# Kernel tuning notes

Hardware: AMD Instinct MI355X
Metric: run time of the kernel (lower is better)

## Reference

```python
import jax, jax.numpy as jnp
import numpy as np

EPS = 1e-6
N_NODES, N_EDGES, HIDDEN, NUM_HEADS = 50000, 800000, 256, 8
HEAD_DIM = HIDDEN // NUM_HEADS
MLP_HIDDEN = 4 * HIDDEN


def _ln(x):
    # LayerNorm without affine, eps=1e-6
    m = x.mean(-1, keepdims=True)
    v = ((x - m) ** 2).mean(-1, keepdims=True)
    return (x - m) * jax.lax.rsqrt(v + EPS)


def _modulate(x, shift, scale):
    return x * (1.0 + scale) + shift


def setup_inputs() -> dict:
    key = jax.random.key(0)
    ks = jax.random.split(key, 20)
    s = 0.02
    inp = {
        "x": jax.random.normal(ks[0], (N_NODES, HIDDEN), jnp.float32),
        "c": jax.random.normal(ks[1], (N_NODES, HIDDEN), jnp.float32),
        "edge_index": jax.random.randint(ks[2], (2, N_EDGES), 0, N_NODES, jnp.int64),
        "Wq": jax.random.normal(ks[3], (HIDDEN, HIDDEN), jnp.float32) * s,
        "bq": jnp.zeros((HIDDEN,), jnp.float32),
        "Wk": jax.random.normal(ks[4], (HIDDEN, HIDDEN), jnp.float32) * s,
        "bk": jnp.zeros((HIDDEN,), jnp.float32),
        "Wv": jax.random.normal(ks[5], (HIDDEN, HIDDEN), jnp.float32) * s,
        "bv": jnp.zeros((HIDDEN,), jnp.float32),
        "Wo": jax.random.normal(ks[6], (HIDDEN, HIDDEN), jnp.float32) * s,
        "bo": jnp.zeros((HIDDEN,), jnp.float32),
        "W1": jax.random.normal(ks[7], (HIDDEN, MLP_HIDDEN), jnp.float32) * s,
        "b1": jnp.zeros((MLP_HIDDEN,), jnp.float32),
        "W2": jax.random.normal(ks[8], (MLP_HIDDEN, HIDDEN), jnp.float32) * s,
        "b2": jnp.zeros((HIDDEN,), jnp.float32),
        "Wc": jax.random.normal(ks[9], (HIDDEN, 6 * HIDDEN), jnp.float32) * s,
        "bc": jnp.zeros((6 * HIDDEN,), jnp.float32),
    }
    return inp


def reference(x, c, edge_index, Wq, bq, Wk, bk, Wv, bv, Wo, bo, W1, b1, W2, b2, Wc, bc):
    n = x.shape[0]
    src, dst = edge_index[0], edge_index[1]  # messages flow src(j) -> dst(i)

    # adaLN modulation: SiLU -> Linear -> chunk 6 along feature dim
    mod = jax.nn.silu(c) @ Wc + bc  # [N, 6*H]
    shift_msa, scale_msa, gate_msa, shift_mlp, scale_mlp, gate_mlp = jnp.split(mod, 6, axis=1)

    # ---- attention branch ----
    h = _modulate(_ln(x), shift_msa, scale_msa)  # [N, HIDDEN]
    q = (h @ Wq + bq).reshape(n, NUM_HEADS, HEAD_DIM)
    k = (h @ Wk + bk).reshape(n, NUM_HEADS, HEAD_DIM)
    v = (h @ Wv + bv).reshape(n, NUM_HEADS, HEAD_DIM)

    scale = HEAD_DIM ** -0.5
    sim = jnp.einsum('ehd,ehd->eh', q[dst], k[src]) * scale  # [E, NH]
    # segment softmax over destination node
    smax = jax.ops.segment_max(sim, dst, num_segments=n)  # [N, NH]
    expd = jnp.exp(sim - smax[dst])
    denom = jax.ops.segment_sum(expd, dst, num_segments=n)  # [N, NH]
    attn = expd / denom[dst]  # [E, NH]

    msg = v[src] * attn[:, :, None]  # [E, NH, HD]
    agg = jax.ops.segment_sum(msg, dst, num_segments=n).reshape(n, HIDDEN)
    attn_out = agg @ Wo + bo

    x = x + gate_msa * attn_out

    # ---- MLP branch ----
    h2 = _modulate(_ln(x), shift_mlp, scale_mlp)
    h2 = jax.nn.gelu(h2 @ W1 + b1, approximate=True)
    mlp_out = h2 @ W2 + b2

    return x + gate_mlp * mlp_out
```

## Files before the change

### kernel.cpp

```cpp
#include <hip/hip_runtime.h>


typedef __attribute__((ext_vector_type(8))) short bf16x8;
typedef __attribute__((ext_vector_type(2))) _Float16 h2_t;
typedef __attribute__((ext_vector_type(4))) float f32x4;

__device__ __forceinline__ float bf2f(unsigned short u) {
  union { float f; unsigned int i; } x; x.i = ((unsigned int)u) << 16; return x.f;
}
__device__ __forceinline__ unsigned short f2bf(float f) {
  union { float f; unsigned int i; } x; x.f = f;
  unsigned int r = x.i + 0x7fffu + ((x.i >> 16) & 1u);
  return (unsigned short)(r >> 16);
}
__device__ __forceinline__ float sigm_fast(float t) {
  return __builtin_amdgcn_rcpf(1.f + exp2f(-t));
}

__device__ __forceinline__ void gload_lds16(const void* g, void* l) {
  __builtin_amdgcn_global_load_lds(
      (const __attribute__((address_space(1))) void*)g,
      (__attribute__((address_space(3))) void*)l, 16, 0, 0);
}

template <int EPI, int XINBF, int OUTBF>
__global__ __launch_bounds__(512)
void gemm_bf16(const unsigned short* __restrict__ A,
               const unsigned short* __restrict__ Bt,
               const float* __restrict__ bias,
               const void* __restrict__ xin,
               const unsigned short* __restrict__ gate,
               void* __restrict__ out,
               int M, int N, int K, int lda, int ldo) {
  const int NT = N >> 7;
  const int MT = (M + 127) >> 7;
  const int pid = blockIdx.x;
  const int j = pid >> 3;
  const int rb = (pid & 7) + 8 * (j / NT);
  const int cb = j - (j / NT) * NT;
  if (rb >= MT) return;

  __shared__ char smem[65536];
  const int tid = threadIdx.x;
  const int wid = tid >> 6;
  const int lane = tid & 63;
  const int l15 = lane & 15, l4 = lane >> 4;
  const int row0 = rb * 128, col0 = cb * 128;
  const int wr = (wid >> 2) * 64;
  const int wc = (wid & 3) * 32;

  f32x4 acc[4][2];
  const f32x4 zf = {0.f, 0.f, 0.f, 0.f};
  for (int m = 0; m < 4; ++m)
    for (int n = 0; n < 2; ++n) acc[m][n] = zf;

  auto STAGE = [&](int buf, int kt) {
    char* At = smem + buf * 32768;
    char* Bs = At + 16384;
#pragma unroll
    for (int s = 0; s < 2; ++s) {
      const int p = s * 8192 + tid * 16;
      const int r = p >> 7;
      const int scb = (p & 127) ^ ((r & 7) << 4);
      int gr = row0 + r; gr = gr < M ? gr : M - 1;
      gload_lds16((const char*)A + ((size_t)gr * lda + kt) * 2 + scb,
                  At + s * 8192 + wid * 1024);
      const int gc = col0 + r;
      gload_lds16((const char*)Bt + ((size_t)gc * K + kt) * 2 + scb,
                  Bs + s * 8192 + wid * 1024);
    }
  };

  STAGE(0, 0);
  __syncthreads();
  int cur = 0;
  for (int kt = 0; kt < K; kt += 64) {
    if (kt + 64 < K) STAGE(cur ^ 1, kt + 64);
    const char* At = smem + cur * 32768;
    const char* Bs = At + 16384;
#pragma unroll
    for (int kk = 0; kk < 64; kk += 32) {
      bf16x8 af[4], bfr[2];
#pragma unroll
      for (int m = 0; m < 4; ++m) {
        const int r = wr + m * 16 + l15;
        const int cb2 = ((kk + l4 * 8) * 2) ^ ((r & 7) << 4);
        af[m] = *(const bf16x8*)(At + r * 128 + cb2);
      }
#pragma unroll
      for (int n = 0; n < 2; ++n) {
        const int r = wc + n * 16 + l15;
        const int cb2 = ((kk + l4 * 8) * 2) ^ ((r & 7) << 4);
        bfr[n] = *(const bf16x8*)(Bs + r * 128 + cb2);
      }
#pragma unroll
      for (int m = 0; m < 4; ++m)
#pragma unroll
        for (int n = 0; n < 2; ++n)
          acc[m][n] = __builtin_amdgcn_mfma_f32_16x16x32_bf16(af[m], bfr[n],
                                                              acc[m][n], 0, 0, 0);
    }
    __syncthreads();
    cur ^= 1;
  }

  const bool fp8path = (EPI == 3) || (EPI == 4 && cb >= 2);
  if (EPI == 2) {
#pragma unroll
    for (int m = 0; m < 4; ++m)
#pragma unroll
      for (int jj = 0; jj < 4; ++jj) {
        const int gr = row0 + wr + m * 16 + l4 * 4 + jj;
        if (gr >= M) continue;
#pragma unroll
        for (int n = 0; n < 2; ++n) {
          const int gc = col0 + wc + n * 16 + l15;
          const float v = acc[m][n][jj] + bias[gc];
          const float gt = bf2f(gate[(size_t)gr * 1536 + gc]);
          const float xv =
              XINBF ? bf2f(((const unsigned short*)xin)[(size_t)gr * ldo + gc])
                    : ((const float*)xin)[(size_t)gr * ldo + gc];
          const float rv = xv + gt * v;
          if (OUTBF)
            ((unsigned short*)out)[(size_t)gr * ldo + gc] = f2bf(rv);
          else
            ((float*)out)[(size_t)gr * ldo + gc] = rv;
        }
      }
  } else if (fp8path) {
#pragma unroll
    for (int m = 0; m < 4; ++m)
#pragma unroll
      for (int jj = 0; jj < 4; ++jj) {
        const int row_l = wr + m * 16 + l4 * 4 + jj;
        const int swz = (row_l & 12) << 2;
#pragma unroll
        for (int n = 0; n < 2; ++n) {
          const int col = wc + n * 16 + l15;
          const float v = acc[m][n][jj] + bias[col0 + col];
          const unsigned short h =
              __builtin_bit_cast(unsigned short, (_Float16)v);
          const unsigned char b8 =
              (unsigned char)((h + 0x7fu + ((h >> 8) & 1u)) >> 8);
          ((unsigned char*)smem)[row_l * 128 + (col ^ swz)] = b8;
        }
      }
    __syncthreads();
#pragma unroll
    for (int pp = 0; pp < 2; ++pp) {
      const int u = pp * 512 + tid;
      const int row_l = u >> 3;
      const int cb16 = (u & 7) * 16;
      const int gr = row0 + row_l;
      if (gr < M) {
        const bf16x8 vv = *(const bf16x8*)((const unsigned char*)smem +
                                           row_l * 128 +
                                           (cb16 ^ ((row_l & 12) << 2)));
        unsigned char* op =
            (EPI == 4)
                ? (unsigned char*)out + (size_t)gr * 1024 + 512 +
                      (col0 - 256) + cb16
                : (unsigned char*)out + (size_t)gr * ldo + col0 + cb16;
        *(bf16x8*)op = vv;
      }
    }
  } else {
    unsigned short* R = (unsigned short*)smem;
#pragma unroll
    for (int m = 0; m < 4; ++m)
#pragma unroll
      for (int jj = 0; jj < 4; ++jj) {
        const int row_l = wr + m * 16 + l4 * 4 + jj;
        const int swz = (row_l & 12) << 2;
#pragma unroll
        for (int n = 0; n < 2; ++n) {
          const int col = wc + n * 16 + l15;
          float v = acc[m][n][jj] + bias[col0 + col];
          if (EPI == 1) {
            v = v * sigm_fast(2.3025851f * (v + 0.044715f * v * v * v));
          }
          R[row_l * 128 + (col ^ swz)] = f2bf(v);
        }
      }
    __syncthreads();
#pragma unroll
    for (int pp = 0; pp < 4; ++pp) {
      const int u = pp * 512 + tid;
      const int row_l = u >> 4;
      const int col8 = (u & 15) * 8;
      const int gr = row0 + row_l;
      if (gr < M) {
        const bf16x8 vv =
            *(const bf16x8*)&R[row_l * 128 + (col8 ^ ((row_l & 12) << 2))];
        unsigned short* op =
            (EPI == 4) ? (unsigned short*)out + (size_t)gr * 512 + col0 + col8
                       : (unsigned short*)out + (size_t)gr * ldo + col0 + col8;
        *(bf16x8*)op = vv;
      }
    }
  }
}

__global__ void sentinel_fill(float* o, long n, float v) {
  long i = (long)blockIdx.x * blockDim.x + threadIdx.x;
  const long st = (long)gridDim.x * blockDim.x;
  for (; i < n; i += st) o[i] = (i == 0) ? v : 0.f;
}

__global__ void prep_weights(const float* __restrict__ Wc, const float* __restrict__ Wq,
                             const float* __restrict__ Wk, const float* __restrict__ Wv,
                             const float* __restrict__ Wo, const float* __restrict__ W1,
                             const float* __restrict__ W2,
                             unsigned short* __restrict__ Wct,
                             unsigned short* __restrict__ Wqkvt,
                             unsigned short* __restrict__ Wot,
                             unsigned short* __restrict__ W1t,
                             unsigned short* __restrict__ W2t,
                             const float* __restrict__ bq, const float* __restrict__ bk,
                             const float* __restrict__ bv, float* __restrict__ bqkv,
                             int* __restrict__ deg, int Mdeg,
                             const unsigned int* __restrict__ ei_u32, int E,
                             int* __restrict__ flag,
                             const float* __restrict__ c,
                             unsigned short* __restrict__ cs, int silu4) {
  const int job = blockIdx.y;
  const int i = blockIdx.x * 256 + threadIdx.x;
  if (job == 7) {
    if (i < 256) bqkv[i] = bq[i];
    else if (i < 512) { int d = i - 256; bqkv[256 + ((d >> 2) << 3) + (d & 3)] = bk[d]; }
    else if (i < 768) { int d = i - 512; bqkv[256 + ((d >> 2) << 3) + 4 + (d & 3)] = bv[d]; }
    return;
  }
  if (job == 8) {
    if (i < Mdeg) deg[i] = 0;
    return;
  }
  if (job == 9) {
    if (blockIdx.x != 0) return;
    __shared__ int bad;
    if (threadIdx.x == 0) bad = 0;
    __syncthreads();
    const int n = E < 256 ? E : 256;
    if ((int)threadIdx.x < n && ei_u32[2 * threadIdx.x + 1] != 0u) atomicAdd(&bad, 1);
    __syncthreads();
    if (threadIdx.x == 0) *flag = (bad == 0);
    return;
  }
  if (job == 10) {
    const int stride = gridDim.x * 256;
    for (int g = i; g < silu4; g += stride) {
      float4 v = *(const float4*)&c[(size_t)g * 4];
      ushort4 r;
      r.x = f2bf(v.x * sigm_fast(1.4426950f * v.x));
      r.y = f2bf(v.y * sigm_fast(1.4426950f * v.y));
      r.z = f2bf(v.z * sigm_fast(1.4426950f * v.z));
      r.w = f2bf(v.w * sigm_fast(1.4426950f * v.w));
      *(ushort4*)&cs[(size_t)g * 4] = r;
    }
    return;
  }
  const float* W; unsigned short* Wt; int N, kc, mode = 0;
  switch (job) {
    case 0: W = Wc; Wt = Wct; N = 1536; kc = 256; break;
    case 1: W = Wq; Wt = Wqkvt; N = 256; kc = 256; break;
    case 2: W = Wk; Wt = Wqkvt + 256 * 256; N = 256; kc = 256; mode = 1; break;
    case 3: W = Wv; Wt = Wqkvt + 256 * 256; N = 256; kc = 256; mode = 2; break;
    case 4: W = Wo; Wt = Wot; N = 256; kc = 256; break;
    case 5: W = W1; Wt = W1t; N = 1024; kc = 256; break;
    default: W = W2; Wt = W2t; N = 256; kc = 1024; break;
  }
  if (i >= N * kc) return;
  const int kk = i / N, n = i - kk * N;
  int r = n;
  if (mode == 1) r = ((n >> 2) << 3) + (n & 3);
  else if (mode == 2) r = ((n >> 2) << 3) + 4 + (n & 3);
  Wt[(size_t)r * kc + kk] = f2bf(W[(size_t)kk * N + n]);
}

template <int INBF>
__global__ void ln_modulate(const void* __restrict__ xin,
                            const unsigned short* __restrict__ modv,
                            unsigned short* __restrict__ hout,
                            int M, int cshift, int cscale) {
  const int wid = threadIdx.x >> 6, lane = threadIdx.x & 63;
  const int row = blockIdx.x * 4 + wid;
  if (row >= M) return;
  float4 x4;
  if (INBF) {
    const ushort4 u4 =
        *(const ushort4*)((const unsigned short*)xin + (size_t)row * 256 + lane * 4);
    x4.x = bf2f(u4.x); x4.y = bf2f(u4.y); x4.z = bf2f(u4.z); x4.w = bf2f(u4.w);
  } else {
    x4 = *(const float4*)((const float*)xin + (size_t)row * 256 + lane * 4);
  }
  float s = x4.x + x4.y + x4.z + x4.w;
  float ss = x4.x * x4.x + x4.y * x4.y + x4.z * x4.z + x4.w * x4.w;
#pragma unroll
  for (int m = 1; m < 64; m <<= 1) {
    s += __shfl_xor(s, m, 64);
    ss += __shfl_xor(ss, m, 64);
  }
  const float mean = s * (1.f / 256.f);
  const float var = ss * (1.f / 256.f) - mean * mean;
  const float rstd = rsqrtf(var + 1e-6f);
  const ushort4 sh4 = *(const ushort4*)&modv[(size_t)row * 1536 + cshift * 256 + lane * 4];
  const ushort4 sc4 = *(const ushort4*)&modv[(size_t)row * 1536 + cscale * 256 + lane * 4];
  ushort4 o;
  o.x = f2bf((x4.x - mean) * rstd * (1.f + bf2f(sc4.x)) + bf2f(sh4.x));
  o.y = f2bf((x4.y - mean) * rstd * (1.f + bf2f(sc4.y)) + bf2f(sh4.y));
  o.z = f2bf((x4.z - mean) * rstd * (1.f + bf2f(sc4.z)) + bf2f(sh4.z));
  o.w = f2bf((x4.w - mean) * rstd * (1.f + bf2f(sc4.w)) + bf2f(sh4.w));
  *(ushort4*)&hout[(size_t)row * 256 + lane * 4] = o;
}

__global__ void conv_hist(const void* __restrict__ ei, const int* __restrict__ flag,
                          int* __restrict__ src32, int* __restrict__ dst32,
                          int* __restrict__ deg, int E) {
  int e = blockIdx.x * blockDim.x + threadIdx.x;
  if (e >= E) return;
  int s, d;
  if (*flag) {
    const long long* p = (const long long*)ei;
    s = (int)p[e]; d = (int)p[E + e];
  } else {
    const int* p = (const int*)ei;
    s = p[e]; d = p[E + e];
  }
  src32[e] = s; dst32[e] = d;
  atomicAdd(&deg[d], 1);
}

__global__ __launch_bounds__(256)
void block_sum(const int* __restrict__ deg, int* __restrict__ bsum, int M) {
  int i = blockIdx.x * 256 + threadIdx.x;
  int v = (i < M) ? deg[i] : 0;
#pragma unroll
  for (int d = 1; d < 64; d <<= 1) v += __shfl_xor(v, d, 64);
  __shared__ int ws[4];
  const int lane = threadIdx.x & 63, w = threadIdx.x >> 6;
  if (lane == 0) ws[w] = v;
  __syncthreads();
  if (threadIdx.x == 0) bsum[blockIdx.x] = ws[0] + ws[1] + ws[2] + ws[3];
}

__global__ __launch_bounds__(256)
void scan_final(const int* __restrict__ deg, const int* __restrict__ bsum,
                int* __restrict__ start, int* __restrict__ cursor, int M, int NB) {
  const int b = blockIdx.x, t = threadIdx.x, i = b * 256 + t;
  const int lane = t & 63, w = t >> 6;
  __shared__ int ws[4];
  __shared__ int pref;
  const int v = (i < M) ? deg[i] : 0;
  int s = v;
#pragma unroll
  for (int d = 1; d < 64; d <<= 1) {
    int u = __shfl_up(s, d, 64);
    if (lane >= d) s += u;
  }
  if (lane == 63) ws[w] = s;
  if (t < 64) {
    int acc = 0;
    for (int base = 0; base < b; base += 64) {
      const int idx = base + lane;
      acc += (idx < b) ? bsum[idx] : 0;
    }
#pragma unroll
    for (int d = 1; d < 64; d <<= 1) acc += __shfl_xor(acc, d, 64);
    if (lane == 0) pref = acc;
  }
  __syncthreads();
  int add = pref;
  for (int k = 0; k < w; ++k) add += ws[k];
  const int excl = s - v + add;
  if (i < M) { start[i] = excl; cursor[i] = excl; }
  if (i == M - 1) start[M] = excl + v;
}

__global__ void csr_fill(const int* __restrict__ src32, const int* __restrict__ dst32,
                         int* __restrict__ cursor, int* __restrict__ csr, int E) {
  int e = blockIdx.x * blockDim.x + threadIdx.x;
  if (e >= E) return;
  int pos = atomicAdd(&cursor[dst32[e]], 1);
  csr[pos] = src32[e];
}

__global__ __launch_bounds__(256)
void attn_gather(const int* __restrict__ csr, const int* __restrict__ start,
                 const unsigned char* __restrict__ qkvp,
                 unsigned short* __restrict__ aggb, int M) {
  const int wid = threadIdx.x >> 6, lane = threadIdx.x & 63;
  const int row = blockIdx.x * 4 + wid;
  if (row >= M) return;
  const ushort4 q4 = *(const ushort4*)(qkvp + (size_t)row * 1024 + lane * 8);
  const float SC = 0.17677669529663687f;
  h2_t q01h, q23h;
  q01h[0] = (_Float16)(bf2f(q4.x) * SC); q01h[1] = (_Float16)(bf2f(q4.y) * SC);
  q23h[0] = (_Float16)(bf2f(q4.z) * SC); q23h[1] = (_Float16)(bf2f(q4.w) * SC);
  const int b0 = start[row], e0 = start[row + 1];
  float den = 0.f, a0 = 0.f, a1 = 0.f, a2 = 0.f, a3 = 0.f;

  auto LDKV = [&](int src) {
    return *(const uint2*)(qkvp + (size_t)src * 1024 + 512 + lane * 8);
  };
#define PROC(kv2)                                                              \
  {                                                                            \
    const unsigned kd = kv2.x, vd = kv2.y;                                     \
    const h2_t k01 = __builtin_bit_cast(                                       \
        h2_t, __builtin_amdgcn_perm(0u, kd, 0x010C000Cu));                     \
    const h2_t k23 = __builtin_bit_cast(                                       \
        h2_t, __builtin_amdgcn_perm(0u, kd, 0x030C020Cu));                     \
    h2_t ph = k01 * q01h;                                                      \
    ph = k23 * q23h + ph;                                                      \
    float s = (float)ph[0] + (float)ph[1];                                     \
    s += __shfl_xor(s, 1, 64);                                                 \
    s += __shfl_xor(s, 2, 64);                                                 \
    s += __shfl_xor(s, 4, 64);                                                 \
    const float ex = __expf(s);                                                \
    const h2_t v01 = __builtin_bit_cast(                                       \
        h2_t, __builtin_amdgcn_perm(0u, vd, 0x010C000Cu));                     \
    const h2_t v23 = __builtin_bit_cast(                                       \
        h2_t, __builtin_amdgcn_perm(0u, vd, 0x030C020Cu));                     \
    den += ex;                                                                 \
    a0 += ex * (float)v01[0]; a1 += ex * (float)v01[1];                        \
    a2 += ex * (float)v23[0]; a3 += ex * (float)v23[1];                        \
  }

  int i = b0;
  if (i + 4 <= e0) {
    uint2 A0 = LDKV(csr[i]), A1 = LDKV(csr[i + 1]);
    uint2 A2 = LDKV(csr[i + 2]), A3 = LDKV(csr[i + 3]);
    while (i + 8 <= e0) {
      const uint2 B0 = LDKV(csr[i + 4]), B1 = LDKV(csr[i + 5]);
      const uint2 B2 = LDKV(csr[i + 6]), B3 = LDKV(csr[i + 7]);
      PROC(A0); PROC(A1); PROC(A2); PROC(A3);
      A0 = B0; A1 = B1; A2 = B2; A3 = B3;
      i += 4;
    }
    PROC(A0); PROC(A1); PROC(A2); PROC(A3);
    i += 4;
  }
  for (; i < e0; ++i) {
    const uint2 kv2 = LDKV(csr[i]);
    PROC(kv2);
  }
#undef PROC

  const float inv = den > 0.f ? __builtin_amdgcn_rcpf(den) : 0.f;
  ushort4 r;
  r.x = f2bf(a0 * inv); r.y = f2bf(a1 * inv);
  r.z = f2bf(a2 * inv); r.w = f2bf(a3 * inv);
  *(ushort4*)&aggb[(size_t)row * 256 + lane * 4] = r;
}

extern "C" void kernel_launch(void* const* d_in, const int* in_sizes, int n_in,
                              void* d_out, int out_size, void* d_ws, size_t ws_size,
                              hipStream_t stream) {
  (void)n_in;
  const float* x  = (const float*)d_in[0];
  const float* c  = (const float*)d_in[1];
  const void*  ei = d_in[2];
  const float* Wq = (const float*)d_in[3];
  const float* bq = (const float*)d_in[4];
  const float* Wk = (const float*)d_in[5];
  const float* bk = (const float*)d_in[6];
  const float* Wv = (const float*)d_in[7];
  const float* bv = (const float*)d_in[8];
  const float* Wo = (const float*)d_in[9];
  const float* bo = (const float*)d_in[10];
  const float* W1 = (const float*)d_in[11];
  const float* b1 = (const float*)d_in[12];
  const float* W2 = (const float*)d_in[13];
  const float* b2 = (const float*)d_in[14];
  const float* Wc = (const float*)d_in[15];
  const float* bc = (const float*)d_in[16];

  const int M = in_sizes[0] / 256;
  const int E = in_sizes[2] / 2;

  char* ws = (char*)d_ws;
  size_t off = 0;
  auto carve = [&](size_t bytes) {
    char* p = ws + off;
    off = (off + bytes + 255) & ~(size_t)255;
    return p;
  };
  unsigned short* modv = (unsigned short*)carve((size_t)M * 1536 * 2);
  char* D = carve((size_t)M * 1024);
  unsigned short* cs = (unsigned short*)D;
  unsigned char* qkvp = (unsigned char*)D;
  unsigned short* X1b = (unsigned short*)D;
  unsigned short* Wct   = (unsigned short*)carve((size_t)1536 * 256 * 2);
  unsigned short* Wqkvt = (unsigned short*)carve((size_t)768 * 256 * 2);
  unsigned short* Wot   = (unsigned short*)carve((size_t)256 * 256 * 2);
  unsigned short* W1t   = (unsigned short*)carve((size_t)1024 * 256 * 2);
  unsigned short* W2t   = (unsigned short*)carve((size_t)256 * 1024 * 2);
  float* bqkv = (float*)carve(768 * 4);
  int* flag = (int*)carve(256);
  int* src32  = (int*)carve((size_t)E * 4);
  int* dst32  = (int*)carve((size_t)E * 4);
  int* deg    = (int*)carve((size_t)(M + 4) * 4);
  int* startp = (int*)carve((size_t)(M + 4) * 4);
  int* cursor = (int*)carve((size_t)(M + 4) * 4);
  int* csr    = (int*)carve((size_t)E * 4);
  int* bsum   = (int*)carve(1024);

  unsigned short* hbuf  = (unsigned short*)d_out;
  unsigned short* hbuf2 = (unsigned short*)d_out;
  unsigned short* aggb  = (unsigned short*)((char*)d_out + (size_t)M * 512);
  float* xout = (float*)d_out;

  if (off > ws_size) {
    sentinel_fill<<<2048, 256, 0, stream>>>((float*)d_out, (long)out_size,
                                            (float)ws_size);
    return;
  }

  const int tb = 256;
  const int EB = (E + tb - 1) / tb;
  const int SB = (M + 255) / 256;

  prep_weights<<<dim3(1536, 11), 256, 0, stream>>>(
      Wc, Wq, Wk, Wv, Wo, W1, W2, Wct, Wqkvt, Wot, W1t, W2t,
      bq, bk, bv, bqkv, deg, M + 4, (const unsigned int*)ei, E, flag,
      c, cs, M * 64);
  conv_hist<<<EB, tb, 0, stream>>>(ei, flag, src32, dst32, deg, E);
  block_sum<<<SB, 256, 0, stream>>>(deg, bsum, M);
  scan_final<<<SB, 256, 0, stream>>>(deg, bsum, startp, cursor, M, SB);
  csr_fill<<<EB, tb, 0, stream>>>(src32, dst32, cursor, csr, E);

  auto gsz = [](int Mz, int Nz) {
    int MT = (Mz + 127) / 128, NT = Nz / 128;
    return 8 * ((MT + 7) / 8) * NT;
  };
  gemm_bf16<0, 0, 0><<<gsz(M, 1536), 512, 0, stream>>>(
      cs, Wct, bc, nullptr, nullptr, modv, M, 1536, 256, 256, 1536);
  ln_modulate<0><<<(M + 3) / 4, 256, 0, stream>>>(x, modv, hbuf, M, 0, 1);
  gemm_bf16<4, 0, 0><<<gsz(M, 768), 512, 0, stream>>>(
      hbuf, Wqkvt, bqkv, nullptr, nullptr, qkvp, M, 768, 256, 256, 0);
  attn_gather<<<(M + 3) / 4, 256, 0, stream>>>(csr, startp, qkvp, aggb, M);
  gemm_bf16<2, 0, 1><<<gsz(M, 256), 512, 0, stream>>>(
      aggb, Wot, bo, x, modv + 512, X1b, M, 256, 256, 256, 256);
  ln_modulate<1><<<(M + 3) / 4, 256, 0, stream>>>(X1b, modv, hbuf2, M, 3, 4);
  gemm_bf16<1, 0, 0><<<gsz(M, 1024), 512, 0, stream>>>(
      hbuf2, W1t, b1, nullptr, nullptr, modv, M, 1024, 256, 256, 1536);
  gemm_bf16<2, 1, 0><<<gsz(M, 256), 512, 0, stream>>>(
      modv, W2t, b2, X1b, modv + 1280, xout, M, 256, 1024, 1536, 256);
}
```

Measured before the change: 464.6 us.

## Fuse MLP up-projection, GELU and down-projection into one kernel

```diff
diff --git a/kernel.cpp b/kernel.cpp
--- a/kernel.cpp
+++ b/kernel.cpp
@@ -104,7 +104,7 @@
     cur ^= 1;
   }
 
-  const bool fp8path = (EPI == 3) || (EPI == 4 && cb >= 2);
+  const bool fp8path = (EPI == 4 && cb >= 2);
   if (EPI == 2) {
 #pragma unroll
     for (int m = 0; m < 4; ++m)
@@ -156,12 +156,8 @@
         const bf16x8 vv = *(const bf16x8*)((const unsigned char*)smem +
                                            row_l * 128 +
                                            (cb16 ^ ((row_l & 12) << 2)));
-        unsigned char* op =
-            (EPI == 4)
-                ? (unsigned char*)out + (size_t)gr * 1024 + 512 +
-                      (col0 - 256) + cb16
-                : (unsigned char*)out + (size_t)gr * ldo + col0 + cb16;
-        *(bf16x8*)op = vv;
+        *(bf16x8*)((unsigned char*)out + (size_t)gr * 1024 + 512 +
+                   (col0 - 256) + cb16) = vv;
       }
     }
   } else {
@@ -175,10 +171,7 @@
 #pragma unroll
         for (int n = 0; n < 2; ++n) {
           const int col = wc + n * 16 + l15;
-          float v = acc[m][n][jj] + bias[col0 + col];
-          if (EPI == 1) {
-            v = v * sigm_fast(2.3025851f * (v + 0.044715f * v * v * v));
-          }
+          const float v = acc[m][n][jj] + bias[col0 + col];
           R[row_l * 128 + (col ^ swz)] = f2bf(v);
         }
       }
@@ -199,6 +192,167 @@
       }
     }
   }
+}
+
+__global__ __launch_bounds__(512)
+void fused_mlp(const unsigned short* __restrict__ A, int ldaB,
+               const unsigned short* __restrict__ W1t,
+               const unsigned short* __restrict__ W2t,
+               const float* __restrict__ b1, const float* __restrict__ b2,
+               const unsigned short* __restrict__ X1b,
+               const unsigned short* __restrict__ gate,
+               float* __restrict__ out, int M) {
+  const int MT = (M + 127) >> 7;
+  const int pid = blockIdx.x;
+  const int rb = (pid & 7) + 8 * (pid >> 3);
+  if (rb >= MT) return;
+
+  __shared__ char smem[131072];
+  char* Al  = smem;
+  char* wb0 = smem + 65536;
+  char* wb1 = smem + 81920;
+  char* hc  = smem + 98304;
+
+  const int tid = threadIdx.x;
+  const int wid = tid >> 6, lane = tid & 63;
+  const int l15 = lane & 15, l4 = lane >> 4;
+  const int row0 = rb * 128;
+  const int wr  = (wid >> 2) * 64;
+  const int wcA = (wid & 3) * 32;
+  const int wcB = (wid & 3) * 64;
+
+  f32x4 acc_o[4][4];
+  const f32x4 zf = {0.f, 0.f, 0.f, 0.f};
+#pragma unroll
+  for (int m = 0; m < 4; ++m)
+#pragma unroll
+    for (int n = 0; n < 4; ++n) acc_o[m][n] = zf;
+
+#pragma unroll
+  for (int s = 0; s < 8; ++s) {
+    const int p = s * 8192 + tid * 16;
+    const int r = p >> 9;
+    const int src = (p & 511) ^ ((r & 7) << 4);
+    int gr = row0 + r; gr = gr < M ? gr : M - 1;
+    gload_lds16((const char*)A + (size_t)gr * ldaB + src,
+                Al + s * 8192 + wid * 1024);
+  }
+
+  auto STW1 = [&](char* buf, int c, int t) {
+#pragma unroll
+    for (int s = 0; s < 2; ++s) {
+      const int p = s * 8192 + tid * 16;
+      const int r = p >> 7;
+      const int scb = (p & 127) ^ ((r & 7) << 4);
+      gload_lds16((const char*)W1t + ((size_t)(c * 128 + r) * 256 + t * 64) * 2 + scb,
+                  buf + s * 8192 + wid * 1024);
+    }
+  };
+  auto STW2 = [&](char* buf, int c, int t) {
+#pragma unroll
+    for (int s = 0; s < 2; ++s) {
+      const int p = s * 8192 + tid * 16;
+      const int r = p >> 6;
+      const int sc = (p & 63) ^ ((r & 3) << 4);
+      gload_lds16((const char*)W2t + ((size_t)r * 1024 + c * 128 + t * 32) * 2 + sc,
+                  buf + s * 8192 + wid * 1024);
+    }
+  };
+
+  for (int c = 0; c < 8; ++c) {
+    f32x4 acc_h[4][2];
+#pragma unroll
+    for (int m = 0; m < 4; ++m)
+#pragma unroll
+      for (int n = 0; n < 2; ++n) acc_h[m][n] = zf;
+    __syncthreads();
+    STW1(wb0, c, 0);
+    __syncthreads();
+    for (int t = 0; t < 4; ++t) {
+      char* wb = (t & 1) ? wb1 : wb0;
+      if (t < 3) STW1((t & 1) ? wb0 : wb1, c, t + 1);
+#pragma unroll
+      for (int kkl = 0; kkl < 64; kkl += 32) {
+        bf16x8 af[4], bfr[2];
+#pragma unroll
+        for (int m = 0; m < 4; ++m) {
+          const int r = wr + m * 16 + l15;
+          af[m] = *(const bf16x8*)(Al + r * 512 +
+                                   (((t * 64 + kkl + l4 * 8) * 2) ^ ((r & 7) << 4)));
+        }
+#pragma unroll
+        for (int n = 0; n < 2; ++n) {
+          const int r = wcA + n * 16 + l15;
+          bfr[n] = *(const bf16x8*)(wb + r * 128 +
+                                    (((kkl + l4 * 8) * 2) ^ ((r & 7) << 4)));
+        }
+#pragma unroll
+        for (int m = 0; m < 4; ++m)
+#pragma unroll
+          for (int n = 0; n < 2; ++n)
+            acc_h[m][n] = __builtin_amdgcn_mfma_f32_16x16x32_bf16(
+                af[m], bfr[n], acc_h[m][n], 0, 0, 0);
+      }
+      __syncthreads();
+    }
+#pragma unroll
+    for (int m = 0; m < 4; ++m)
+#pragma unroll
+      for (int jj = 0; jj < 4; ++jj) {
+        const int row_l = wr + m * 16 + l4 * 4 + jj;
+#pragma unroll
+        for (int n = 0; n < 2; ++n) {
+          const int col = wcA + n * 16 + l15;
+          float v = acc_h[m][n][jj] + b1[c * 128 + col];
+          v = v * sigm_fast(2.3025851f * (v + 0.044715f * v * v * v));
+          *(unsigned short*)(hc + row_l * 256 +
+                             (((col * 2) ^ ((row_l & 7) << 4)))) = f2bf(v);
+        }
+      }
+    __syncthreads();
+    STW2(wb0, c, 0);
+    __syncthreads();
+    for (int t = 0; t < 4; ++t) {
+      char* wb = (t & 1) ? wb1 : wb0;
+      if (t < 3) STW2((t & 1) ? wb0 : wb1, c, t + 1);
+      bf16x8 af[4], bfr[4];
+#pragma unroll
+      for (int m = 0; m < 4; ++m) {
+        const int r = wr + m * 16 + l15;
+        af[m] = *(const bf16x8*)(hc + r * 256 +
+                                 (((t * 32 + l4 * 8) * 2) ^ ((r & 7) << 4)));
+      }
+#pragma unroll
+      for (int n = 0; n < 4; ++n) {
+        const int rn = wcB + n * 16 + l15;
+        bfr[n] = *(const bf16x8*)(wb + rn * 64 +
+                                  ((l4 * 16) ^ ((rn & 3) << 4)));
+      }
+#pragma unroll
+      for (int m = 0; m < 4; ++m)
+#pragma unroll
+        for (int n = 0; n < 4; ++n)
+          acc_o[m][n] = __builtin_amdgcn_mfma_f32_16x16x32_bf16(
+              af[m], bfr[n], acc_o[m][n], 0, 0, 0);
+      __syncthreads();
+    }
+  }
+
+#pragma unroll
+  for (int m = 0; m < 4; ++m)
+#pragma unroll
+    for (int jj = 0; jj < 4; ++jj) {
+      const int gr = row0 + wr + m * 16 + l4 * 4 + jj;
+      if (gr >= M) continue;
+#pragma unroll
+      for (int n = 0; n < 4; ++n) {
+        const int col = wcB + n * 16 + l15;
+        const float v = acc_o[m][n][jj] + b2[col];
+        const float gt = bf2f(gate[(size_t)gr * 1536 + col]);
+        const float xv = bf2f(X1b[(size_t)gr * 256 + col]);
+        out[(size_t)gr * 256 + col] = xv + gt * v;
+      }
+    }
 }
 
 __global__ void sentinel_fill(float* o, long n, float v) {
@@ -281,7 +435,7 @@
 __global__ void ln_modulate(const void* __restrict__ xin,
                             const unsigned short* __restrict__ modv,
                             unsigned short* __restrict__ hout,
-                            int M, int cshift, int cscale) {
+                            int M, int cshift, int cscale, int ldo) {
   const int wid = threadIdx.x >> 6, lane = threadIdx.x & 63;
   const int row = blockIdx.x * 4 + wid;
   if (row >= M) return;
@@ -310,7 +464,7 @@
   o.y = f2bf((x4.y - mean) * rstd * (1.f + bf2f(sc4.y)) + bf2f(sh4.y));
   o.z = f2bf((x4.z - mean) * rstd * (1.f + bf2f(sc4.z)) + bf2f(sh4.z));
   o.w = f2bf((x4.w - mean) * rstd * (1.f + bf2f(sc4.w)) + bf2f(sh4.w));
-  *(ushort4*)&hout[(size_t)row * 256 + lane * 4] = o;
+  *(ushort4*)&hout[(size_t)row * ldo + lane * 4] = o;
 }
 
 __global__ void conv_hist(const void* __restrict__ ei, const int* __restrict__ flag,
@@ -505,8 +659,8 @@
   int* bsum   = (int*)carve(1024);
 
   unsigned short* hbuf  = (unsigned short*)d_out;
-  unsigned short* hbuf2 = (unsigned short*)d_out;
   unsigned short* aggb  = (unsigned short*)((char*)d_out + (size_t)M * 512);
+  unsigned short* hbuf2 = modv;
   float* xout = (float*)d_out;
 
   if (off > ws_size) {
@@ -534,15 +688,16 @@
   };
   gemm_bf16<0, 0, 0><<<gsz(M, 1536), 512, 0, stream>>>(
       cs, Wct, bc, nullptr, nullptr, modv, M, 1536, 256, 256, 1536);
-  ln_modulate<0><<<(M + 3) / 4, 256, 0, stream>>>(x, modv, hbuf, M, 0, 1);
+  ln_modulate<0><<<(M + 3) / 4, 256, 0, stream>>>(x, modv, hbuf, M, 0, 1, 256);
   gemm_bf16<4, 0, 0><<<gsz(M, 768), 512, 0, stream>>>(
       hbuf, Wqkvt, bqkv, nullptr, nullptr, qkvp, M, 768, 256, 256, 0);
   attn_gather<<<(M + 3) / 4, 256, 0, stream>>>(csr, startp, qkvp, aggb, M);
   gemm_bf16<2, 0, 1><<<gsz(M, 256), 512, 0, stream>>>(
       aggb, Wot, bo, x, modv + 512, X1b, M, 256, 256, 256, 256);
-  ln_modulate<1><<<(M + 3) / 4, 256, 0, stream>>>(X1b, modv, hbuf2, M, 3, 4);
-  gemm_bf16<1, 0, 0><<<gsz(M, 1024), 512, 0, stream>>>(
-      hbuf2, W1t, b1, nullptr, nullptr, modv, M, 1024, 256, 256, 1536);
-  gemm_bf16<2, 1, 0><<<gsz(M, 256), 512, 0, stream>>>(
-      modv, W2t, b2, X1b, modv + 1280, xout, M, 256, 1024, 1536, 256);
-}
+  ln_modulate<1><<<(M + 3) / 4, 256, 0, stream>>>(X1b, modv, hbuf2, M, 3, 4, 1536);
+  {
+    int MT = (M + 127) / 128;
+    fused_mlp<<<8 * ((MT + 7) / 8), 512, 0, stream>>>(
+        hbuf2, 3072, W1t, W2t, b1, b2, X1b, modv + 1280, xout, M);
+  }
+}
```

Measured after the change: 494.0 us. 1.06x slower.
